# Kernel tuning notes

Hardware: AMD Instinct MI355X
Metric: run time of the kernel (lower is better)

The kernel has to match this reference:

```python
import jax, jax.numpy as jnp
import numpy as np

R = 16
N = 524288          # hash table size per level
F = 2               # features per entry
MIN_RES, MAX_RES = 16, 2048
PRIME = 2654435761  # spatial hash prime (as in the torch module)
H = R * F           # MLP width = 32
M = 1048576         # number of query points

# resolutions exactly as in NGP.__init__
RESOLUTIONS = np.round(
    np.logspace(np.log2(MIN_RES), np.log2(MAX_RES), R, base=2)
).astype(np.float32)


def setup_inputs() -> dict:
    key = jax.random.key(0)
    ks = jax.random.split(key, 8)
    coords = jax.random.uniform(ks[0], (M, 2), dtype=jnp.float32)
    hash_features = jax.random.normal(ks[1], (R, N, F), dtype=jnp.float32)
    s = 1.0 / np.sqrt(H)
    W0 = jax.random.uniform(ks[2], (H, H), dtype=jnp.float32, minval=-s, maxval=s)
    b0 = jax.random.uniform(ks[3], (H,), dtype=jnp.float32, minval=-s, maxval=s)
    W1 = jax.random.uniform(ks[4], (H, H), dtype=jnp.float32, minval=-s, maxval=s)
    b1 = jax.random.uniform(ks[5], (H,), dtype=jnp.float32, minval=-s, maxval=s)
    W2 = jax.random.uniform(ks[6], (H, 3), dtype=jnp.float32, minval=-s, maxval=s)
    b2 = jax.random.uniform(ks[7], (3,), dtype=jnp.float32, minval=-s, maxval=s)
    return {"coords": coords, "hash_features": hash_features,
            "W0": W0, "b0": b0, "W1": W1, "b1": b1, "W2": W2, "b2": b2}


def _bilerp_hash(coords, hash_features):
    """coords [M,2] in [0,1); hash_features [R,N,F] -> [M, R*F]."""
    res = jnp.asarray(RESOLUTIONS)  # [R]
    prime = jnp.uint32(PRIME)
    n = jnp.uint32(N)

    def level(res_r, table_r):  # table_r: [N,F]
        x = coords * res_r                    # [M,2]
        xf = jnp.floor(x)
        w = x - xf                            # bilinear weights [M,2]
        xi = xf.astype(jnp.uint32)
        x0, y0 = xi[:, 0], xi[:, 1]

        def look(xx, yy):
            idx = (xx ^ (prime * yy)) % n     # spatial hash
            return table_r[idx]               # gather [M,F]

        wx, wy = w[:, :1], w[:, 1:]
        return (look(x0, y0) * (1 - wx) * (1 - wy)
                + look(x0, y0 + 1) * (1 - wx) * wy
                + look(x0 + 1, y0) * wx * (1 - wy)
                + look(x0 + 1, y0 + 1) * wx * wy)  # [M,F]

    feats = jax.vmap(level)(res, hash_features)   # [R,M,F]
    return jnp.transpose(feats, (1, 0, 2)).reshape(coords.shape[0], -1)  # [M,R*F]


def reference(coords, hash_features, W0, b0, W1, b1, W2, b2):
    f = _bilerp_hash(coords, hash_features)          # [M, 32]
    h = jax.nn.leaky_relu(f @ W0 + b0, 0.01)
    h = jax.nn.leaky_relu(h @ W1 + b1, 0.01)
    return h @ W2 + b2                               # [M, 3]
```

## Files before the change

kernel.cpp:

```cpp
#include <hip/hip_runtime.h>
#include <cmath>

#define R_LEVELS 16
#define N_TAB    524288u
#define N_MASK   (N_TAB - 1u)
#define PRIME_H  2654435761u
#define M_PTS    1048576
#define BDIM     128
#define NBUCK    (BDIM * BDIM)
#define SBLK     64
#define STHR     1024
#define SPB      (M_PTS / SBLK)
#define SITER    (SPB / STHR)
#define XSTRIDE  36
#define NFRAG    384

typedef __attribute__((ext_vector_type(8)))  short bf16x8;
typedef __attribute__((ext_vector_type(16))) float f32x16;

union FragU { bf16x8 v; uint4 q; unsigned u[4]; uint2 u2[2]; unsigned short s[8]; };

struct ResArr { float r[R_LEVELS]; };

__device__ __forceinline__ unsigned pack_hi(float f0, float f1) {
    return __builtin_amdgcn_perm(__float_as_uint(f1), __float_as_uint(f0), 0x07060302u);
}
__device__ __forceinline__ unsigned pack_lo(float f0, float f1) {
    const float l0 = f0 - __uint_as_float(__float_as_uint(f0) & 0xffff0000u);
    const float l1 = f1 - __uint_as_float(__float_as_uint(f1) & 0xffff0000u);
    unsigned r;
    asm("v_cvt_pk_bf16_f32 %0, %1, %2" : "=v"(r) : "v"(l0), "v"(l1));
    return r;
}

__device__ __forceinline__ unsigned bucket_of(float x, float y) {
    unsigned bx = (unsigned)(x * (float)BDIM); if (bx >= BDIM) bx = BDIM - 1;
    unsigned by = (unsigned)(y * (float)BDIM); if (by >= BDIM) by = BDIM - 1;
    unsigned m = 0;
    #pragma unroll
    for (int i = 0; i < 7; ++i)
        m |= (((bx >> i) & 1u) << (2 * i)) | (((by >> i) & 1u) << (2 * i + 1));
    return m;
}

__global__ __launch_bounds__(STHR) void hist_k(const float2* __restrict__ coords,
                                               unsigned short* __restrict__ C) {
    __shared__ unsigned h[NBUCK];
    const int t = threadIdx.x;
    const int w = blockIdx.x;
    #pragma unroll
    for (int i = t; i < NBUCK; i += STHR) h[i] = 0u;
    __syncthreads();
    #pragma unroll
    for (int k = 0; k < SITER; ++k) {
        const int p = w * SPB + k * STHR + t;
        const float2 c = coords[p];
        atomicAdd(&h[bucket_of(c.x, c.y)], 1u);
    }
    __syncthreads();
    #pragma unroll
    for (int i = t; i < NBUCK; i += STHR)
        C[(size_t)w * NBUCK + i] = (unsigned short)h[i];
}

__global__ __launch_bounds__(256) void scanw_k(unsigned short* __restrict__ C,
                                               unsigned* __restrict__ T) {
    const int b = blockIdx.x * 256 + threadIdx.x;
    unsigned s = 0;
    for (int w = 0; w < SBLK; ++w) {
        const size_t i = (size_t)w * NBUCK + b;
        const unsigned v = C[i];
        C[i] = (unsigned short)s;
        s += v;
    }
    T[b] = s;
}

__global__ __launch_bounds__(256) void scan_k(const unsigned* __restrict__ T,
                                              unsigned* __restrict__ B) {
    __shared__ unsigned part[256];
    const int t = threadIdx.x;
    unsigned sum = 0;
    for (int k = 0; k < 64; ++k) sum += T[t * 64 + k];
    part[t] = sum;
    __syncthreads();
    for (int off = 1; off < 256; off <<= 1) {
        const unsigned v = (t >= off) ? part[t - off] : 0u;
        __syncthreads();
        part[t] += v;
        __syncthreads();
    }
    unsigned run = (t > 0) ? part[t - 1] : 0u;
    for (int k = 0; k < 64; ++k) {
        B[t * 64 + k] = run;
        run += T[t * 64 + k];
    }
}

__global__ __launch_bounds__(STHR) void scatter_k(const float2* __restrict__ coords,
                                                  const unsigned short* __restrict__ C,
                                                  const unsigned* __restrict__ B,
                                                  unsigned* __restrict__ sidx) {
    __shared__ unsigned off[NBUCK];
    const int t = threadIdx.x;
    const int w = blockIdx.x;
    #pragma unroll
    for (int i = t; i < NBUCK; i += STHR)
        off[i] = B[i] + (unsigned)C[(size_t)w * NBUCK + i];
    __syncthreads();
    #pragma unroll
    for (int k = 0; k < SITER; ++k) {
        const int p = w * SPB + k * STHR + t;
        const float2 c = coords[p];
        const unsigned b = bucket_of(c.x, c.y);
        const unsigned pos = atomicAdd(&off[b], 1u);
        sidx[pos] = (unsigned)p;
    }
}

__global__ __launch_bounds__(64) void wprep_k(const float* __restrict__ W0,
                                              const float* __restrict__ W1,
                                              const float* __restrict__ W2,
                                              const float* __restrict__ b2,
                                              uint4* __restrict__ wbuf,
                                              float* __restrict__ b2p) {
    const int lane = threadIdx.x;
    const int l31 = lane & 31;
    const int h   = lane >> 5;
    const float* Ws[3] = {W0, W1, W2};
    const int ncols[3] = {32, 32, 3};
    for (int l = 0; l < 3; ++l) {
        for (int kc = 0; kc < 2; ++kc) {
            FragU H, L;
            for (int e = 0; e < 8; ++e) {
                const int k = kc*16 + (e>>2)*8 + h*4 + (e&3);
                const float w = (l31 < ncols[l]) ? Ws[l][k*ncols[l] + l31] : 0.f;
                const unsigned short hi = (unsigned short)(__float_as_uint(w) >> 16);
                const float rem = w - __uint_as_float((unsigned)hi << 16);
                const unsigned u = __float_as_uint(rem);
                const unsigned short lo = (unsigned short)((u + 0x7fffu + ((u >> 16) & 1u)) >> 16);
                H.s[e] = hi;
                L.s[e] = lo;
            }
            const int fi = (l*2 + kc)*64 + lane;
            wbuf[fi]         = H.q;
            wbuf[NFRAG + fi] = L.q;
        }
    }
    if (lane < 32) b2p[lane] = (lane < 3) ? b2[lane] : 0.f;
}

__global__ __launch_bounds__(256) void ngp_mfma(
    const float2* __restrict__ coords,
    const unsigned* __restrict__ sidx,
    const float* __restrict__ hashf,
    const uint4* __restrict__ wbuf,
    const float* __restrict__ b0,
    const float* __restrict__ b1,
    const float* __restrict__ b2p,
    float* __restrict__ out, ResArr res)
{
    __shared__ unsigned short Xh[256 * XSTRIDE];
    __shared__ unsigned short Xl[256 * XSTRIDE];

    const unsigned nwg = gridDim.x;
    const unsigned chunk = nwg >> 3;
    const unsigned sb = (blockIdx.x & 7u) * chunk + (blockIdx.x >> 3);
    const int tid = threadIdx.x;
    const int p = (int)(sb * 256u) + tid;

    const unsigned oid = sidx ? sidx[p] : (unsigned)p;
    const float2 c = coords[oid];

    float f[32];
    #pragma unroll
    for (int ck = 0; ck < 2; ++ck) {
        float2 v00[8], v01[8], v10[8], v11[8];
        float wxs[8], wys[8];
        #pragma unroll
        for (int j = 0; j < 8; ++j) {
            const int r = ck * 8 + j;
            const float rr = res.r[r];
            const float x = c.x * rr;
            const float y = c.y * rr;
            const float xf = floorf(x);
            const float yf = floorf(y);
            wxs[j] = x - xf;
            wys[j] = y - yf;
            const unsigned x0 = (unsigned)xf;
            const unsigned y0 = (unsigned)yf;
            const unsigned hy0 = PRIME_H * y0;
            const unsigned hy1 = PRIME_H * (y0 + 1u);
            const unsigned i00 = (x0 ^ hy0) & N_MASK;
            const unsigned i01 = (x0 ^ hy1) & N_MASK;
            const unsigned i10 = ((x0 + 1u) ^ hy0) & N_MASK;
            const unsigned i11 = ((x0 + 1u) ^ hy1) & N_MASK;
            const float2* tab = (const float2*)hashf + (size_t)r * N_TAB;
            v00[j] = tab[i00];
            v01[j] = tab[i01];
            v10[j] = tab[i10];
            v11[j] = tab[i11];
        }
        #pragma unroll
        for (int j = 0; j < 8; ++j) {
            const float wx = wxs[j], wy = wys[j];
            const float w00 = (1.f - wx) * (1.f - wy);
            const float w01 = (1.f - wx) * wy;
            const float w10 = wx * (1.f - wy);
            const float w11 = wx * wy;
            const int r = ck * 8 + j;
            f[2*r+0] = v00[j].x*w00 + v01[j].x*w01 + v10[j].x*w10 + v11[j].x*w11;
            f[2*r+1] = v00[j].y*w00 + v01[j].y*w01 + v10[j].y*w10 + v11[j].y*w11;
        }
    }

    {
        const int rowo = tid * XSTRIDE;
        #pragma unroll
        for (int q = 0; q < 8; ++q) {
            uint2 ph, pl;
            ph.x = pack_hi(f[4*q+0], f[4*q+1]);
            ph.y = pack_hi(f[4*q+2], f[4*q+3]);
            pl.x = pack_lo(f[4*q+0], f[4*q+1]);
            pl.y = pack_lo(f[4*q+2], f[4*q+3]);
            *(uint2*)&Xh[rowo + 4*q] = ph;
            *(uint2*)&Xl[rowo + 4*q] = pl;
        }
    }

    const int lane = tid & 63;
    const int wv   = tid >> 6;
    const int l31  = lane & 31;
    const int h    = lane >> 5;
    const int tb0  = wv * 64;
    const int tb1  = wv * 64 + 32;

    auto ldx = [&](const unsigned short* X, int ptl, int kc) -> bf16x8 {
        FragU r;
        const int off = ptl * XSTRIDE + kc * 16 + h * 4;
        r.u2[0] = *(const uint2*)&X[off];
        r.u2[1] = *(const uint2*)&X[off + 8];
        return r.v;
    };

    auto bias_init = [&](const float* b) -> f32x16 {
        f32x16 a;
        #pragma unroll
        for (int q = 0; q < 4; ++q) {
            const float4 t = *(const float4*)(b + 8*q + 4*h);
            a[4*q+0] = t.x; a[4*q+1] = t.y; a[4*q+2] = t.z; a[4*q+3] = t.w;
        }
        return a;
    };

    auto layer = [&](int l, const float* b, f32x16& a0, f32x16& a1) {
        FragU wh0, wl0, wh1, wl1;
        wh0.q = wbuf[(l*2+0)*64 + lane];
        wl0.q = wbuf[NFRAG + (l*2+0)*64 + lane];
        wh1.q = wbuf[(l*2+1)*64 + lane];
        wl1.q = wbuf[NFRAG + (l*2+1)*64 + lane];
        f32x16 A0 = bias_init(b);
        f32x16 A1 = A0;
        {
            const bf16x8 xh = ldx(Xh, tb0 + l31, 0);
            const bf16x8 xl = ldx(Xl, tb0 + l31, 0);
            A0 = __builtin_amdgcn_mfma_f32_32x32x16_bf16(wh0.v, xh, A0, 0, 0, 0);
            A0 = __builtin_amdgcn_mfma_f32_32x32x16_bf16(wh0.v, xl, A0, 0, 0, 0);
            A0 = __builtin_amdgcn_mfma_f32_32x32x16_bf16(wl0.v, xh, A0, 0, 0, 0);
        }
        {
            const bf16x8 xh = ldx(Xh, tb1 + l31, 0);
            const bf16x8 xl = ldx(Xl, tb1 + l31, 0);
            A1 = __builtin_amdgcn_mfma_f32_32x32x16_bf16(wh0.v, xh, A1, 0, 0, 0);
            A1 = __builtin_amdgcn_mfma_f32_32x32x16_bf16(wh0.v, xl, A1, 0, 0, 0);
            A1 = __builtin_amdgcn_mfma_f32_32x32x16_bf16(wl0.v, xh, A1, 0, 0, 0);
        }
        {
            const bf16x8 xh = ldx(Xh, tb0 + l31, 1);
            const bf16x8 xl = ldx(Xl, tb0 + l31, 1);
            A0 = __builtin_amdgcn_mfma_f32_32x32x16_bf16(wh1.v, xh, A0, 0, 0, 0);
            A0 = __builtin_amdgcn_mfma_f32_32x32x16_bf16(wh1.v, xl, A0, 0, 0, 0);
            A0 = __builtin_amdgcn_mfma_f32_32x32x16_bf16(wl1.v, xh, A0, 0, 0, 0);
        }
        {
            const bf16x8 xh = ldx(Xh, tb1 + l31, 1);
            const bf16x8 xl = ldx(Xl, tb1 + l31, 1);
            A1 = __builtin_amdgcn_mfma_f32_32x32x16_bf16(wh1.v, xh, A1, 0, 0, 0);
            A1 = __builtin_amdgcn_mfma_f32_32x32x16_bf16(wh1.v, xl, A1, 0, 0, 0);
            A1 = __builtin_amdgcn_mfma_f32_32x32x16_bf16(wl1.v, xh, A1, 0, 0, 0);
        }
        a0 = A0; a1 = A1;
    };

    auto store_act = [&](const f32x16& a, int ptl) {
        const int rowo = ptl * XSTRIDE;
        #pragma unroll
        for (int q = 0; q < 4; ++q) {
            float v0 = a[4*q+0], v1 = a[4*q+1], v2 = a[4*q+2], v3 = a[4*q+3];
            v0 = fmaxf(v0, 0.01f*v0);
            v1 = fmaxf(v1, 0.01f*v1);
            v2 = fmaxf(v2, 0.01f*v2);
            v3 = fmaxf(v3, 0.01f*v3);
            uint2 ph, pl;
            ph.x = pack_hi(v0, v1); ph.y = pack_hi(v2, v3);
            pl.x = pack_lo(v0, v1); pl.y = pack_lo(v2, v3);
            const int off = rowo + 8*q + 4*h;
            *(uint2*)&Xh[off] = ph;
            *(uint2*)&Xl[off] = pl;
        }
    };

    f32x16 a0, a1;
    layer(0, b0, a0, a1);
    store_act(a0, tb0 + l31);
    store_act(a1, tb1 + l31);
    layer(1, b1, a0, a1);
    store_act(a0, tb0 + l31);
    store_act(a1, tb1 + l31);
    layer(2, b2p, a0, a1);

    if (h == 0) {
        const int pl0 = (int)(sb * 256u) + tb0 + l31;
        const int pl1 = (int)(sb * 256u) + tb1 + l31;
        const unsigned o0 = sidx ? sidx[pl0] : (unsigned)pl0;
        const unsigned o1 = sidx ? sidx[pl1] : (unsigned)pl1;
        out[(size_t)o0*3 + 0] = a0[0];
        out[(size_t)o0*3 + 1] = a0[1];
        out[(size_t)o0*3 + 2] = a0[2];
        out[(size_t)o1*3 + 0] = a1[0];
        out[(size_t)o1*3 + 1] = a1[1];
        out[(size_t)o1*3 + 2] = a1[2];
    }
}

extern "C" void kernel_launch(void* const* d_in, const int* in_sizes, int n_in,
                              void* d_out, int out_size, void* d_ws, size_t ws_size,
                              hipStream_t stream) {
    ResArr res;
    for (int i = 0; i < R_LEVELS; ++i)
        res.r[i] = (float)nearbyint(exp2(4.0 + (7.0 / 15.0) * (double)i));
    res.r[0] = 16.f;
    res.r[R_LEVELS - 1] = 2048.f;

    const float2* coords = (const float2*)d_in[0];
    const float* hashf   = (const float*)d_in[1];
    const float* W0      = (const float*)d_in[2];
    const float* b0      = (const float*)d_in[3];
    const float* W1      = (const float*)d_in[4];
    const float* b1      = (const float*)d_in[5];
    const float* W2      = (const float*)d_in[6];
    const float* b2      = (const float*)d_in[7];
    float* out           = (float*)d_out;

    const size_t off_C    = 0;
    const size_t off_T    = off_C + (size_t)SBLK * NBUCK * 2;
    const size_t off_B    = off_T + NBUCK * 4;
    const size_t off_sidx = off_B + NBUCK * 4;
    const size_t off_wbuf = off_sidx + (size_t)M_PTS * 4;
    const size_t off_b2p  = off_wbuf + 2 * NFRAG * sizeof(uint4);
    const size_t need     = off_b2p + 32 * sizeof(float);
    const size_t need_min = 2 * NFRAG * sizeof(uint4) + 32 * sizeof(float);

    dim3 blockM(256);
    dim3 gridM(M_PTS / 256);

    if (ws_size >= need) {
        unsigned short* C = (unsigned short*)((char*)d_ws + off_C);
        unsigned* T    = (unsigned*)((char*)d_ws + off_T);
        unsigned* B    = (unsigned*)((char*)d_ws + off_B);
        unsigned* sidx = (unsigned*)((char*)d_ws + off_sidx);
        uint4*    wbuf = (uint4*)((char*)d_ws + off_wbuf);
        float*    b2p  = (float*)((char*)d_ws + off_b2p);

        hipLaunchKernelGGL(wprep_k,   dim3(1), dim3(64), 0, stream, W0, W1, W2, b2, wbuf, b2p);
        hipLaunchKernelGGL(hist_k,    dim3(SBLK), dim3(STHR), 0, stream, coords, C);
        hipLaunchKernelGGL(scanw_k,   dim3(NBUCK / 256), dim3(256), 0, stream, C, T);
        hipLaunchKernelGGL(scan_k,    dim3(1), dim3(256), 0, stream, T, B);
        hipLaunchKernelGGL(scatter_k, dim3(SBLK), dim3(STHR), 0, stream, coords, C, B, sidx);
        hipLaunchKernelGGL(ngp_mfma,  gridM, blockM, 0, stream,
                           coords, sidx, hashf, wbuf, b0, b1, b2p, out, res);
    } else if (ws_size >= need_min) {
        uint4* wbuf = (uint4*)d_ws;
        float* b2p  = (float*)((char*)d_ws + 2 * NFRAG * sizeof(uint4));
        hipLaunchKernelGGL(wprep_k,   dim3(1), dim3(64), 0, stream, W0, W1, W2, b2, wbuf, b2p);
        hipLaunchKernelGGL(ngp_mfma,  gridM, blockM, 0, stream,
                           coords, (const unsigned*)nullptr, hashf, wbuf, b0, b1, b2p, out, res);
    }
}
```

Baseline: 123.3 us.

## Compute hash features directly in MFMA fragment layout and drop LDS staging

Each wave now interpolates only the levels its lanes need for the MFMA B-operand layout, two points per lane split by half-wave, and packs the results straight into register fragments. This removes the shared-memory staging of features and activations between layers. Activations are repacked in registers using the accumulator layout. The scatter pass also writes sorted coordinates so the main kernel reads them contiguously instead of through an indirect gather. The cost is that each thread now issues hash lookups for two points (half the levels each), which raises register pressure, and the scatter kernel writes an extra array.

```diff
diff --git a/kernel.cpp b/kernel.cpp
--- a/kernel.cpp
+++ b/kernel.cpp
@@ -12,13 +12,12 @@
 #define STHR     1024
 #define SPB      (M_PTS / SBLK)
 #define SITER    (SPB / STHR)
-#define XSTRIDE  36
 #define NFRAG    384
 
 typedef __attribute__((ext_vector_type(8)))  short bf16x8;
 typedef __attribute__((ext_vector_type(16))) float f32x16;
 
-union FragU { bf16x8 v; uint4 q; unsigned u[4]; uint2 u2[2]; unsigned short s[8]; };
+union FragU { bf16x8 v; uint4 q; unsigned u[4]; unsigned short s[8]; };
 
 struct ResArr { float r[R_LEVELS]; };
 
@@ -100,6 +99,7 @@
 __global__ __launch_bounds__(STHR) void scatter_k(const float2* __restrict__ coords,
                                                   const unsigned short* __restrict__ C,
                                                   const unsigned* __restrict__ B,
+                                                  float2* __restrict__ sxy,
                                                   unsigned* __restrict__ sidx) {
     __shared__ unsigned off[NBUCK];
     const int t = threadIdx.x;
@@ -114,6 +114,7 @@
         const float2 c = coords[p];
         const unsigned b = bucket_of(c.x, c.y);
         const unsigned pos = atomicAdd(&off[b], 1u);
+        sxy[pos] = c;
         sidx[pos] = (unsigned)p;
     }
 }
@@ -123,7 +124,9 @@
                                               const float* __restrict__ W2,
                                               const float* __restrict__ b2,
                                               uint4* __restrict__ wbuf,
-                                              float* __restrict__ b2p) {
+                                              float* __restrict__ b2p,
+                                              float* __restrict__ restab,
+                                              ResArr res) {
     const int lane = threadIdx.x;
     const int l31 = lane & 31;
     const int h   = lane >> 5;
@@ -148,45 +151,55 @@
         }
     }
     if (lane < 32) b2p[lane] = (lane < 3) ? b2[lane] : 0.f;
+    if (lane < R_LEVELS) restab[lane] = res.r[lane];
 }
 
 __global__ __launch_bounds__(256) void ngp_mfma(
-    const float2* __restrict__ coords,
+    const float2* __restrict__ pts,
     const unsigned* __restrict__ sidx,
     const float* __restrict__ hashf,
     const uint4* __restrict__ wbuf,
     const float* __restrict__ b0,
     const float* __restrict__ b1,
     const float* __restrict__ b2p,
-    float* __restrict__ out, ResArr res)
+    const float* __restrict__ restab,
+    float* __restrict__ out)
 {
-    __shared__ unsigned short Xh[256 * XSTRIDE];
-    __shared__ unsigned short Xl[256 * XSTRIDE];
-
     const unsigned nwg = gridDim.x;
     const unsigned chunk = nwg >> 3;
     const unsigned sb = (blockIdx.x & 7u) * chunk + (blockIdx.x >> 3);
-    const int tid = threadIdx.x;
-    const int p = (int)(sb * 256u) + tid;
-
-    const unsigned oid = sidx ? sidx[p] : (unsigned)p;
-    const float2 c = coords[oid];
-
-    float f[32];
-    #pragma unroll
-    for (int ck = 0; ck < 2; ++ck) {
-        float2 v00[8], v01[8], v10[8], v11[8];
-        float wxs[8], wys[8];
-        #pragma unroll
-        for (int j = 0; j < 8; ++j) {
-            const int r = ck * 8 + j;
-            const float rr = res.r[r];
-            const float x = c.x * rr;
-            const float y = c.y * rr;
+    const int tid  = threadIdx.x;
+    const int lane = tid & 63;
+    const int wv   = tid >> 6;
+    const int l31  = lane & 31;
+    const int h    = lane >> 5;
+    const int base = (int)(sb * 256u) + wv * 64;
+    const int pA   = base + l31;
+    const int pB   = base + 32 + l31;
+
+    const float2 cA = pts[pA];
+    const float2 cB = pts[pB];
+
+    float2 resp[4];
+    #pragma unroll
+    for (int c = 0; c < 4; ++c)
+        resp[c] = *(const float2*)&restab[4*c + 2*h];
+
+    auto interp_half = [&](float2 cc, int half, FragU& H, FragU& L) {
+        float2 v00[4], v01[4], v10[4], v11[4];
+        float wxs[4], wys[4];
+        #pragma unroll
+        for (int q = 0; q < 4; ++q) {
+            const int c = 2*half + (q>>1);
+            const int d = q & 1;
+            const int lvi = 4*c + 2*h + d;
+            const float rr = d ? resp[c].y : resp[c].x;
+            const float x = cc.x * rr;
+            const float y = cc.y * rr;
             const float xf = floorf(x);
             const float yf = floorf(y);
-            wxs[j] = x - xf;
-            wys[j] = y - yf;
+            wxs[q] = x - xf;
+            wys[q] = y - yf;
             const unsigned x0 = (unsigned)xf;
             const unsigned y0 = (unsigned)yf;
             const unsigned hy0 = PRIME_H * y0;
@@ -195,52 +208,24 @@
             const unsigned i01 = (x0 ^ hy1) & N_MASK;
             const unsigned i10 = ((x0 + 1u) ^ hy0) & N_MASK;
             const unsigned i11 = ((x0 + 1u) ^ hy1) & N_MASK;
-            const float2* tab = (const float2*)hashf + (size_t)r * N_TAB;
-            v00[j] = tab[i00];
-            v01[j] = tab[i01];
-            v10[j] = tab[i10];
-            v11[j] = tab[i11];
-        }
-        #pragma unroll
-        for (int j = 0; j < 8; ++j) {
-            const float wx = wxs[j], wy = wys[j];
+            const float2* tab = (const float2*)hashf + ((size_t)lvi << 19);
+            v00[q] = tab[i00];
+            v01[q] = tab[i01];
+            v10[q] = tab[i10];
+            v11[q] = tab[i11];
+        }
+        #pragma unroll
+        for (int q = 0; q < 4; ++q) {
+            const float wx = wxs[q], wy = wys[q];
             const float w00 = (1.f - wx) * (1.f - wy);
             const float w01 = (1.f - wx) * wy;
             const float w10 = wx * (1.f - wy);
             const float w11 = wx * wy;
-            const int r = ck * 8 + j;
-            f[2*r+0] = v00[j].x*w00 + v01[j].x*w01 + v10[j].x*w10 + v11[j].x*w11;
-            f[2*r+1] = v00[j].y*w00 + v01[j].y*w01 + v10[j].y*w10 + v11[j].y*w11;
-        }
-    }
-
-    {
-        const int rowo = tid * XSTRIDE;
-        #pragma unroll
-        for (int q = 0; q < 8; ++q) {
-            uint2 ph, pl;
-            ph.x = pack_hi(f[4*q+0], f[4*q+1]);
-            ph.y = pack_hi(f[4*q+2], f[4*q+3]);
-            pl.x = pack_lo(f[4*q+0], f[4*q+1]);
-            pl.y = pack_lo(f[4*q+2], f[4*q+3]);
-            *(uint2*)&Xh[rowo + 4*q] = ph;
-            *(uint2*)&Xl[rowo + 4*q] = pl;
-        }
-    }
-
-    const int lane = tid & 63;
-    const int wv   = tid >> 6;
-    const int l31  = lane & 31;
-    const int h    = lane >> 5;
-    const int tb0  = wv * 64;
-    const int tb1  = wv * 64 + 32;
-
-    auto ldx = [&](const unsigned short* X, int ptl, int kc) -> bf16x8 {
-        FragU r;
-        const int off = ptl * XSTRIDE + kc * 16 + h * 4;
-        r.u2[0] = *(const uint2*)&X[off];
-        r.u2[1] = *(const uint2*)&X[off + 8];
-        return r.v;
+            const float f0 = v00[q].x*w00 + v01[q].x*w01 + v10[q].x*w10 + v11[q].x*w11;
+            const float f1 = v00[q].y*w00 + v01[q].y*w01 + v10[q].y*w10 + v11[q].y*w11;
+            H.u[q] = pack_hi(f0, f1);
+            L.u[q] = pack_lo(f0, f1);
+        }
     };
 
     auto bias_init = [&](const float* b) -> f32x16 {
@@ -253,7 +238,17 @@
         return a;
     };
 
-    auto layer = [&](int l, const float* b, f32x16& a0, f32x16& a1) {
+    FragU Ah0, Al0, Ah1, Al1;
+    FragU Bh0, Bl0, Bh1, Bl1;
+
+    interp_half(cA, 0, Ah0, Al0);
+    interp_half(cA, 1, Ah1, Al1);
+    interp_half(cB, 0, Bh0, Bl0);
+    interp_half(cB, 1, Bh1, Bl1);
+
+    f32x16 a0, a1;
+
+    auto layer = [&](int l, const float* b) {
         FragU wh0, wl0, wh1, wl1;
         wh0.q = wbuf[(l*2+0)*64 + lane];
         wl0.q = wbuf[NFRAG + (l*2+0)*64 + lane];
@@ -261,69 +256,45 @@
         wl1.q = wbuf[NFRAG + (l*2+1)*64 + lane];
         f32x16 A0 = bias_init(b);
         f32x16 A1 = A0;
-        {
-            const bf16x8 xh = ldx(Xh, tb0 + l31, 0);
-            const bf16x8 xl = ldx(Xl, tb0 + l31, 0);
-            A0 = __builtin_amdgcn_mfma_f32_32x32x16_bf16(wh0.v, xh, A0, 0, 0, 0);
-            A0 = __builtin_amdgcn_mfma_f32_32x32x16_bf16(wh0.v, xl, A0, 0, 0, 0);
-            A0 = __builtin_amdgcn_mfma_f32_32x32x16_bf16(wl0.v, xh, A0, 0, 0, 0);
-        }
-        {
-            const bf16x8 xh = ldx(Xh, tb1 + l31, 0);
-            const bf16x8 xl = ldx(Xl, tb1 + l31, 0);
-            A1 = __builtin_amdgcn_mfma_f32_32x32x16_bf16(wh0.v, xh, A1, 0, 0, 0);
-            A1 = __builtin_amdgcn_mfma_f32_32x32x16_bf16(wh0.v, xl, A1, 0, 0, 0);
-            A1 = __builtin_amdgcn_mfma_f32_32x32x16_bf16(wl0.v, xh, A1, 0, 0, 0);
-        }
-        {
-            const bf16x8 xh = ldx(Xh, tb0 + l31, 1);
-            const bf16x8 xl = ldx(Xl, tb0 + l31, 1);
-            A0 = __builtin_amdgcn_mfma_f32_32x32x16_bf16(wh1.v, xh, A0, 0, 0, 0);
-            A0 = __builtin_amdgcn_mfma_f32_32x32x16_bf16(wh1.v, xl, A0, 0, 0, 0);
-            A0 = __builtin_amdgcn_mfma_f32_32x32x16_bf16(wl1.v, xh, A0, 0, 0, 0);
-        }
-        {
-            const bf16x8 xh = ldx(Xh, tb1 + l31, 1);
-            const bf16x8 xl = ldx(Xl, tb1 + l31, 1);
-            A1 = __builtin_amdgcn_mfma_f32_32x32x16_bf16(wh1.v, xh, A1, 0, 0, 0);
-            A1 = __builtin_amdgcn_mfma_f32_32x32x16_bf16(wh1.v, xl, A1, 0, 0, 0);
-            A1 = __builtin_amdgcn_mfma_f32_32x32x16_bf16(wl1.v, xh, A1, 0, 0, 0);
-        }
+        A0 = __builtin_amdgcn_mfma_f32_32x32x16_bf16(wh0.v, Ah0.v, A0, 0, 0, 0);
+        A0 = __builtin_amdgcn_mfma_f32_32x32x16_bf16(wh0.v, Al0.v, A0, 0, 0, 0);
+        A0 = __builtin_amdgcn_mfma_f32_32x32x16_bf16(wl0.v, Ah0.v, A0, 0, 0, 0);
+        A0 = __builtin_amdgcn_mfma_f32_32x32x16_bf16(wh1.v, Ah1.v, A0, 0, 0, 0);
+        A0 = __builtin_amdgcn_mfma_f32_32x32x16_bf16(wh1.v, Al1.v, A0, 0, 0, 0);
+        A0 = __builtin_amdgcn_mfma_f32_32x32x16_bf16(wl1.v, Ah1.v, A0, 0, 0, 0);
+        A1 = __builtin_amdgcn_mfma_f32_32x32x16_bf16(wh0.v, Bh0.v, A1, 0, 0, 0);
+        A1 = __builtin_amdgcn_mfma_f32_32x32x16_bf16(wh0.v, Bl0.v, A1, 0, 0, 0);
+        A1 = __builtin_amdgcn_mfma_f32_32x32x16_bf16(wl0.v, Bh0.v, A1, 0, 0, 0);
+        A1 = __builtin_amdgcn_mfma_f32_32x32x16_bf16(wh1.v, Bh1.v, A1, 0, 0, 0);
+        A1 = __builtin_amdgcn_mfma_f32_32x32x16_bf16(wh1.v, Bl1.v, A1, 0, 0, 0);
+        A1 = __builtin_amdgcn_mfma_f32_32x32x16_bf16(wl1.v, Bh1.v, A1, 0, 0, 0);
         a0 = A0; a1 = A1;
     };
 
-    auto store_act = [&](const f32x16& a, int ptl) {
-        const int rowo = ptl * XSTRIDE;
-        #pragma unroll
-        for (int q = 0; q < 4; ++q) {
-            float v0 = a[4*q+0], v1 = a[4*q+1], v2 = a[4*q+2], v3 = a[4*q+3];
-            v0 = fmaxf(v0, 0.01f*v0);
-            v1 = fmaxf(v1, 0.01f*v1);
-            v2 = fmaxf(v2, 0.01f*v2);
-            v3 = fmaxf(v3, 0.01f*v3);
-            uint2 ph, pl;
-            ph.x = pack_hi(v0, v1); ph.y = pack_hi(v2, v3);
-            pl.x = pack_lo(v0, v1); pl.y = pack_lo(v2, v3);
-            const int off = rowo + 8*q + 4*h;
-            *(uint2*)&Xh[off] = ph;
-            *(uint2*)&Xl[off] = pl;
+    auto act_repack = [&](const f32x16& a, FragU& xh0, FragU& xl0, FragU& xh1, FragU& xl1) {
+        float v[16];
+        #pragma unroll
+        for (int r = 0; r < 16; ++r) v[r] = fmaxf(a[r], 0.01f * a[r]);
+        #pragma unroll
+        for (int w = 0; w < 4; ++w) {
+            xh0.u[w] = pack_hi(v[2*w],   v[2*w+1]);
+            xl0.u[w] = pack_lo(v[2*w],   v[2*w+1]);
+            xh1.u[w] = pack_hi(v[8+2*w], v[8+2*w+1]);
+            xl1.u[w] = pack_lo(v[8+2*w], v[8+2*w+1]);
         }
     };
 
-    f32x16 a0, a1;
-    layer(0, b0, a0, a1);
-    store_act(a0, tb0 + l31);
-    store_act(a1, tb1 + l31);
-    layer(1, b1, a0, a1);
-    store_act(a0, tb0 + l31);
-    store_act(a1, tb1 + l31);
-    layer(2, b2p, a0, a1);
+    layer(0, b0);
+    act_repack(a0, Ah0, Al0, Ah1, Al1);
+    act_repack(a1, Bh0, Bl0, Bh1, Bl1);
+    layer(1, b1);
+    act_repack(a0, Ah0, Al0, Ah1, Al1);
+    act_repack(a1, Bh0, Bl0, Bh1, Bl1);
+    layer(2, b2p);
 
     if (h == 0) {
-        const int pl0 = (int)(sb * 256u) + tb0 + l31;
-        const int pl1 = (int)(sb * 256u) + tb1 + l31;
-        const unsigned o0 = sidx ? sidx[pl0] : (unsigned)pl0;
-        const unsigned o1 = sidx ? sidx[pl1] : (unsigned)pl1;
+        const unsigned o0 = sidx ? sidx[pA] : (unsigned)pA;
+        const unsigned o1 = sidx ? sidx[pB] : (unsigned)pB;
         out[(size_t)o0*3 + 0] = a0[0];
         out[(size_t)o0*3 + 1] = a0[1];
         out[(size_t)o0*3 + 2] = a0[2];
@@ -352,14 +323,17 @@
     const float* b2      = (const float*)d_in[7];
     float* out           = (float*)d_out;
 
-    const size_t off_C    = 0;
-    const size_t off_T    = off_C + (size_t)SBLK * NBUCK * 2;
-    const size_t off_B    = off_T + NBUCK * 4;
-    const size_t off_sidx = off_B + NBUCK * 4;
-    const size_t off_wbuf = off_sidx + (size_t)M_PTS * 4;
-    const size_t off_b2p  = off_wbuf + 2 * NFRAG * sizeof(uint4);
-    const size_t need     = off_b2p + 32 * sizeof(float);
-    const size_t need_min = 2 * NFRAG * sizeof(uint4) + 32 * sizeof(float);
+    const size_t off_C      = 0;
+    const size_t off_T      = off_C + (size_t)SBLK * NBUCK * 2;
+    const size_t off_B      = off_T + NBUCK * 4;
+    const size_t off_sxy    = off_B + NBUCK * 4;
+    const size_t off_sidx   = off_sxy + (size_t)M_PTS * sizeof(float2);
+    const size_t off_wbuf   = off_sidx + (size_t)M_PTS * 4;
+    const size_t off_b2p    = off_wbuf + 2 * NFRAG * sizeof(uint4);
+    const size_t off_restab = off_b2p + 32 * sizeof(float);
+    const size_t need       = off_restab + R_LEVELS * sizeof(float);
+    const size_t need_min   = 2 * NFRAG * sizeof(uint4) + 32 * sizeof(float)
+                              + R_LEVELS * sizeof(float);
 
     dim3 blockM(256);
     dim3 gridM(M_PTS / 256);
@@ -368,22 +342,27 @@
         unsigned short* C = (unsigned short*)((char*)d_ws + off_C);
         unsigned* T    = (unsigned*)((char*)d_ws + off_T);
         unsigned* B    = (unsigned*)((char*)d_ws + off_B);
+        float2*   sxy  = (float2*)((char*)d_ws + off_sxy);
         unsigned* sidx = (unsigned*)((char*)d_ws + off_sidx);
         uint4*    wbuf = (uint4*)((char*)d_ws + off_wbuf);
         float*    b2p  = (float*)((char*)d_ws + off_b2p);
-
-        hipLaunchKernelGGL(wprep_k,   dim3(1), dim3(64), 0, stream, W0, W1, W2, b2, wbuf, b2p);
+        float*    rtab = (float*)((char*)d_ws + off_restab);
+
+        hipLaunchKernelGGL(wprep_k,   dim3(1), dim3(64), 0, stream,
+                           W0, W1, W2, b2, wbuf, b2p, rtab, res);
         hipLaunchKernelGGL(hist_k,    dim3(SBLK), dim3(STHR), 0, stream, coords, C);
         hipLaunchKernelGGL(scanw_k,   dim3(NBUCK / 256), dim3(256), 0, stream, C, T);
         hipLaunchKernelGGL(scan_k,    dim3(1), dim3(256), 0, stream, T, B);
-        hipLaunchKernelGGL(scatter_k, dim3(SBLK), dim3(STHR), 0, stream, coords, C, B, sidx);
+        hipLaunchKernelGGL(scatter_k, dim3(SBLK), dim3(STHR), 0, stream, coords, C, B, sxy, sidx);
         hipLaunchKernelGGL(ngp_mfma,  gridM, blockM, 0, stream,
-                           coords, sidx, hashf, wbuf, b0, b1, b2p, out, res);
+                           sxy, sidx, hashf, wbuf, b0, b1, b2p, rtab, out);
     } else if (ws_size >= need_min) {
         uint4* wbuf = (uint4*)d_ws;
         float* b2p  = (float*)((char*)d_ws + 2 * NFRAG * sizeof(uint4));
-        hipLaunchKernelGGL(wprep_k,   dim3(1), dim3(64), 0, stream, W0, W1, W2, b2, wbuf, b2p);
+        float* rtab = b2p + 32;
+        hipLaunchKernelGGL(wprep_k,   dim3(1), dim3(64), 0, stream,
+                           W0, W1, W2, b2, wbuf, b2p, rtab, res);
         hipLaunchKernelGGL(ngp_mfma,  gridM, blockM, 0, stream,
-                           coords, (const unsigned*)nullptr, hashf, wbuf, b0, b1, b2p, out, res);
-    }
-}
+                           coords, (const unsigned*)nullptr, hashf, wbuf, b0, b1, b2p, rtab, out);
+    }
+}
```

New measurement: 141.3 us. 14.5% more time.
